# Kernel tuning notes

Hardware: AMD Instinct MI355X
Metric: run time of the kernel (lower is better)

The kernel has to match this reference:

```python
import jax, jax.numpy as jnp
import numpy as np

L0, L1, L2 = 32, 16, 8          # multiplicities of 0e, 1o, 2e irreps
NS = 128                        # numscalars
NB = 64                         # numbasis
CUTOFF = 7.0
N_NODES = 50000
N_EDGES = 400000
N_GRAPH = 32
NODE_DIM = L0 + 3 * L1 + 5 * L2  # 120


def setup_inputs() -> dict:
    key = jax.random.key(0)
    ks = jax.random.split(key, 16)
    return {
        "nodes": jax.random.normal(ks[0], (N_NODES, NODE_DIM), jnp.float32),
        "edge_index": jax.random.randint(ks[1], (2, N_EDGES), 0, N_NODES),
        "graph_batch": jnp.sort(jax.random.randint(ks[2], (N_NODES,), 0, N_GRAPH)),
        "cell": jax.random.normal(ks[3], (N_GRAPH, 3, 3), jnp.float32),
        "edge_shift": jax.random.normal(ks[4], (N_EDGES, 3), jnp.float32),
        "pos": jax.random.normal(ks[5], (N_NODES, 3), jnp.float32),
        # FullyConnectedTensorProduct weights: one uvw block per (l,l)->0e path
        "W0": jax.random.normal(ks[6], (L0, L0, NS), jnp.float32),
        "W1": jax.random.normal(ks[7], (L1, L1, NS), jnp.float32),
        "W2": jax.random.normal(ks[8], (L2, L2, NS), jnp.float32),
        "ln_g": jnp.ones((NS,), jnp.float32),
        "ln_b": jnp.zeros((NS,), jnp.float32),
        "df_w1": jax.random.normal(ks[9], (NB, 128), jnp.float32) / np.sqrt(NB).astype(np.float32),
        "df_b1": jnp.zeros((128,), jnp.float32),
        "df_w2": jax.random.normal(ks[10], (128, NS), jnp.float32) / np.sqrt(128.0).astype(np.float32),
        "df_b2": jnp.zeros((NS,), jnp.float32),
        "mlp_w1": jax.random.normal(ks[11], (NS, 512), jnp.float32) / np.sqrt(NS).astype(np.float32),
        "mlp_b1": jnp.zeros((512,), jnp.float32),
        "mlp_w2": jax.random.normal(ks[12], (512, 1), jnp.float32) / np.sqrt(512.0).astype(np.float32),
        "mlp_b2": jnp.zeros((1,), jnp.float32),
    }


def _split_irreps(x):
    # x: [E, L0 + 3*L1 + 5*L2] -> scalar / vector / rank-2 blocks
    a = x[:, :L0]                                   # [E, L0]    0e
    b = x[:, L0:L0 + 3 * L1].reshape(-1, L1, 3)     # [E, L1, 3] 1o
    c = x[:, L0 + 3 * L1:].reshape(-1, L2, 5)       # [E, L2, 5] 2e
    return a, b, c


def _tensor_product(x1, x2, W0, W1, W2):
    # e3nn FullyConnectedTensorProduct to {NS}x0e: only (l,l)->0 paths survive.
    # Real-basis wigner_3j(l,l,0) = I / sqrt(2l+1); 'element' path norm with
    # scalar output gives alpha = 1 / (L0^2 + L1^2 + L2^2) shared by all paths.
    a1, b1, c1 = _split_irreps(x1)
    a2, b2, c2 = _split_irreps(x2)
    alpha = 1.0 / np.sqrt(float(L0 * L0 + L1 * L1 + L2 * L2))
    out = (jnp.einsum('eu,ev,uvw->ew', a1, a2, W0)
           + jnp.einsum('eum,evm,uvw->ew', b1, b2, W1) * (1.0 / np.sqrt(3.0))
           + jnp.einsum('eum,evm,uvw->ew', c1, c2, W2) * (1.0 / np.sqrt(5.0)))
    return jnp.asarray(alpha, out.dtype) * out


def reference(nodes, edge_index, graph_batch, cell, edge_shift, pos,
              W0, W1, W2, ln_g, ln_b, df_w1, df_b1, df_w2, df_b2,
              mlp_w1, mlp_b1, mlp_w2, mlp_b2):
    src, dst = edge_index[0], edge_index[1]
    bcell = cell[graph_batch[src]]                            # [E,3,3]
    tvec = jnp.einsum('ei,eij->ej', edge_shift, bcell)        # [E,3]
    radvec = pos[dst] - pos[src] + tvec
    dist = jnp.linalg.norm(radvec, axis=1, keepdims=True)     # [E,1]

    mixed = _tensor_product(nodes[src], nodes[dst], W0, W1, W2)  # [E,NS]
    mu = jnp.mean(mixed, axis=-1, keepdims=True)
    var = jnp.mean((mixed - mu) ** 2, axis=-1, keepdims=True)
    mixednorm = (mixed - mu) / jnp.sqrt(var + 1e-5) * ln_g + ln_b

    # RadialEmbedding: Gaussian RBF * cosine envelope with hard cutoff
    offset = jnp.linspace(0.0, CUTOFF, NB).astype(dist.dtype)
    width = CUTOFF / (NB - 1)
    coeff = -0.5 / (width * width)
    rbf = jnp.exp(coeff * (dist - offset[None, :]) ** 2)      # [E,NB]
    env = 0.5 * (jnp.cos(dist * jnp.pi / CUTOFF) + 1.0)
    env = env * (dist < CUTOFF).astype(dist.dtype)            # [E,1]
    demb = rbf * env

    dfilter = jax.nn.silu(demb @ df_w1 + df_b1) @ df_w2 + df_b2  # [E,NS]
    regulated = mixednorm * dfilter
    out = jax.nn.silu(regulated @ mlp_w1 + mlp_b1) @ mlp_w2 + mlp_b2  # [E,1]
    return out
```

## Files before the change

kernel.cpp:

```cpp
#include <hip/hip_runtime.h>
#include <hip/hip_bf16.h>
#include <math.h>

typedef unsigned short ushort_t;
typedef short short8 __attribute__((ext_vector_type(8)));
typedef float f32x4 __attribute__((ext_vector_type(4)));

#define E_TOTAL 400000
#define ET 32
#define NTHR 512
#define NODE_D 120
#define XSTR 124

#define ALPHA 0.0272772362793f
#define S_L1  0.57735026918962f
#define S_L2  0.44721359549996f

#define WS_WF1 172032
#define WS_WF2 180224
#define WS_WM1 196608
#define WS_TOTAL 262144

__device__ __forceinline__ ushort_t f2b(float f) {
    unsigned int b = __float_as_uint(f);
    b += 0x7FFFu + ((b >> 16) & 1u);
    return (ushort_t)(b >> 16);
}
__device__ __forceinline__ unsigned int f2b2(float a, float b) {
    __hip_bfloat162 h = __float22bfloat162_rn(make_float2(a, b));
    union { __hip_bfloat162 h2; unsigned int u; } cv; cv.h2 = h;
    return cv.u;
}
__device__ __forceinline__ float silu_f(float x) { return x / (1.0f + __expf(-x)); }

__global__ __launch_bounds__(256) void prep_weights(
    const float* __restrict__ W0, const float* __restrict__ W1, const float* __restrict__ W2,
    const float* __restrict__ df_w1, const float* __restrict__ df_w2,
    const float* __restrict__ mlp_w1, ushort_t* __restrict__ ws)
{
    const int i = blockIdx.x * 256 + threadIdx.x;
    if (i >= WS_TOTAL) return;
    float v;
    if (i < WS_WF1) {
        const int r = i;
        const int kt = r >> 12, nt = (r >> 9) & 7, l = (r >> 3) & 63, jj = r & 7;
        const int k = kt * 32 + ((l >> 4) << 3) + jj;
        const int n = nt * 16 + (l & 15);
        if (k < 1024)      v = W0[k * 128 + n] * ALPHA;
        else if (k < 1280) v = W1[(k - 1024) * 128 + n] * (ALPHA * S_L1);
        else               v = W2[(k - 1280) * 128 + n] * (ALPHA * S_L2);
    } else if (i < WS_WF2) {
        const int r = i - WS_WF1;
        const int kt = r >> 12, nt = (r >> 9) & 7, l = (r >> 3) & 63, jj = r & 7;
        v = df_w1[(kt * 32 + ((l >> 4) << 3) + jj) * 128 + nt * 16 + (l & 15)];
    } else if (i < WS_WM1) {
        const int r = i - WS_WF2;
        const int kt = r >> 12, nt = (r >> 9) & 7, l = (r >> 3) & 63, jj = r & 7;
        v = df_w2[(kt * 32 + ((l >> 4) << 3) + jj) * 128 + nt * 16 + (l & 15)];
    } else {
        const int r = i - WS_WM1;
        const int kt = r >> 14, nt = (r >> 9) & 31, l = (r >> 3) & 63, jj = r & 7;
        v = mlp_w1[(kt * 32 + ((l >> 4) << 3) + jj) * 512 + nt * 16 + (l & 15)];
    }
    ws[i] = f2b(v);
}

__device__ __forceinline__ void build_l0_frag(ushort_t* __restrict__ Pf,
                                              const float* __restrict__ x1,
                                              const float* __restrict__ x2,
                                              int tid, int ubase)
{
    const int er = tid & 15, kg = (tid >> 4) & 3, w = tid >> 6;
#pragma unroll
    for (int half = 0; half < 2; ++half) {
        const int e = half * 16 + er;
        const float* x2r = x2 + e * XSTR + kg * 8;
        const float2 xv0 = *(const float2*)(x2r + 0);
        const float2 xv1 = *(const float2*)(x2r + 2);
        const float2 xv2 = *(const float2*)(x2r + 4);
        const float2 xv3 = *(const float2*)(x2r + 6);
#pragma unroll
        for (int uu = 0; uu < 2; ++uu) {
            const int ul = w + uu * 8;
            const float a1 = x1[e * XSTR + ubase + ul];
            uint4 o;
            o.x = f2b2(a1 * xv0.x, a1 * xv0.y);
            o.y = f2b2(a1 * xv1.x, a1 * xv1.y);
            o.z = f2b2(a1 * xv2.x, a1 * xv2.y);
            o.w = f2b2(a1 * xv3.x, a1 * xv3.y);
            *(uint4*)(Pf + ((ul * 2 + half) * 64 + kg * 16 + er) * 8) = o;
        }
    }
}

__global__ __launch_bounds__(NTHR, 4) void fused_edge_kernel(
    const float* __restrict__ nodes, const int* __restrict__ edge_index,
    const int* __restrict__ graph_batch, const float* __restrict__ cell,
    const float* __restrict__ edge_shift, const float* __restrict__ pos,
    const float* __restrict__ ln_g, const float* __restrict__ ln_b,
    const float* __restrict__ df_b1, const float* __restrict__ df_b2,
    const float* __restrict__ mlp_b1, const float* __restrict__ mlp_w2,
    const float* __restrict__ mlp_b2,
    const ushort_t* __restrict__ wsp, float* __restrict__ out)
{
    __shared__ __align__(16) ushort_t Pf[16 * 2 * 64 * 8];
    __shared__ __align__(16) float xbuf[2 * ET * XSTR];
    __shared__ __align__(16) ushort_t dembF[2 * 2 * 64 * 8];
    __shared__ float dist_s[ET];
    __shared__ int sidx[ET], didx[ET];
    __shared__ float mu_s[ET], rstd_s[ET];

    float* x1 = xbuf;
    float* x2 = xbuf + ET * XSTR;
    ushort_t* h1F  = (ushort_t*)xbuf;
    ushort_t* regF = (ushort_t*)xbuf + 4096;
    float* red1 = (float*)((char*)xbuf + 16384);
    float* red2 = (float*)((char*)xbuf + 18432);

    const int tid = threadIdx.x;
    const int e0g = blockIdx.x * ET;
    const int wave = tid >> 6, lane = tid & 63;
    const int lr = lane & 15, lg = lane >> 4;

    if (tid < ET) {
        const int e = e0g + tid;
        const int s = edge_index[e];
        const int d = edge_index[E_TOTAL + e];
        sidx[tid] = s; didx[tid] = d;
        const int g = graph_batch[s];
        const float* c = cell + g * 9;
        const float sx = edge_shift[e * 3], sy = edge_shift[e * 3 + 1], sz = edge_shift[e * 3 + 2];
        const float t0 = sx * c[0] + sy * c[3] + sz * c[6];
        const float t1 = sx * c[1] + sy * c[4] + sz * c[7];
        const float t2 = sx * c[2] + sy * c[5] + sz * c[8];
        const float r0 = pos[d * 3 + 0] - pos[s * 3 + 0] + t0;
        const float r1 = pos[d * 3 + 1] - pos[s * 3 + 1] + t1;
        const float r2 = pos[d * 3 + 2] - pos[s * 3 + 2] + t2;
        dist_s[tid] = sqrtf(r0 * r0 + r1 * r1 + r2 * r2);
    }
    __syncthreads();

    for (int i = tid; i < ET * 32; i += NTHR) {
        const int e = i >> 5, c = i & 31;
        if (c < 30)
            *(float4*)(x1 + e * XSTR + c * 4) = *(const float4*)(nodes + (size_t)sidx[e] * NODE_D + c * 4);
    }
    for (int i = tid; i < ET * 32; i += NTHR) {
        const int e = i >> 5, c = i & 31;
        if (c < 30)
            *(float4*)(x2 + e * XSTR + c * 4) = *(const float4*)(nodes + (size_t)didx[e] * NODE_D + c * 4);
    }
    for (int i = tid; i < ET * 64; i += NTHR) {
        const int e = i >> 6, k = i & 63;
        const float d = dist_s[e];
        const float t = d - (7.0f / 63.0f) * (float)k;
        const float rbf = __expf(-40.5f * t * t);
        const float env = (d < 7.0f) ? (0.5f * (__cosf(d * (3.14159265358979f / 7.0f)) + 1.0f)) : 0.0f;
        const int ktl = k >> 5, kg = (k >> 3) & 3, jj = k & 7, half = e >> 4, row = e & 15;
        dembF[((ktl * 2 + half) * 64 + kg * 16 + row) * 8 + jj] = f2b(rbf * env);
    }
    __syncthreads();

    const char* pA = (const char*)Pf + lane * 16;
    const short8* WT8 = (const short8*)wsp;
    const int bcol = wave * 64 + lane;

    f32x4 acc0 = {0.f, 0.f, 0.f, 0.f}, acc1 = {0.f, 0.f, 0.f, 0.f};

    build_l0_frag(Pf, x1, x2, tid, 0);
    __syncthreads();
#pragma unroll 4
    for (int kt = 0; kt < 16; ++kt) {
        const short8 a0 = *(const short8*)(pA + kt * 2048);
        const short8 a1 = *(const short8*)(pA + kt * 2048 + 1024);
        const short8 b = WT8[kt * 512 + bcol];
        acc0 = __builtin_amdgcn_mfma_f32_16x16x32_bf16(a0, b, acc0, 0, 0, 0);
        acc1 = __builtin_amdgcn_mfma_f32_16x16x32_bf16(a1, b, acc1, 0, 0, 0);
    }
    __syncthreads();

    build_l0_frag(Pf, x1, x2, tid, 16);
    __syncthreads();
#pragma unroll 4
    for (int kt = 0; kt < 16; ++kt) {
        const short8 a0 = *(const short8*)(pA + kt * 2048);
        const short8 a1 = *(const short8*)(pA + kt * 2048 + 1024);
        const short8 b = WT8[(16 + kt) * 512 + bcol];
        acc0 = __builtin_amdgcn_mfma_f32_16x16x32_bf16(a0, b, acc0, 0, 0, 0);
        acc1 = __builtin_amdgcn_mfma_f32_16x16x32_bf16(a1, b, acc1, 0, 0, 0);
    }
    __syncthreads();

    {
        const int er = tid & 15, kg = (tid >> 4) & 3, w = tid >> 6;
        const int u1 = 2 * w + (kg >> 1);
        const int vb = (kg & 1) * 8;
#pragma unroll
        for (int half = 0; half < 2; ++half) {
            const int e = half * 16 + er;
            const float* b1p = x1 + e * XSTR + 32 + 3 * u1;
            const float b1a = b1p[0], b1b = b1p[1], b1c = b1p[2];
            const float* b2b = x2 + e * XSTR + 32 + 3 * vb;
            float pr[8];
#pragma unroll
            for (int jj = 0; jj < 8; ++jj) {
                const float* b2p = b2b + 3 * jj;
                pr[jj] = b1a * b2p[0] + b1b * b2p[1] + b1c * b2p[2];
            }
            uint4 o;
            o.x = f2b2(pr[0], pr[1]); o.y = f2b2(pr[2], pr[3]);
            o.z = f2b2(pr[4], pr[5]); o.w = f2b2(pr[6], pr[7]);
            *(uint4*)(Pf + ((w * 2 + half) * 64 + lane) * 8) = o;
        }
        if (w < 4) {
            const int half = w & 1;
            const int ktl = 8 + (w >> 1);
            const int u2 = (ktl - 8) * 4 + kg;
            const int e = half * 16 + er;
            const float* c1p = x1 + e * XSTR + 80 + 5 * u2;
            const float c1a = c1p[0], c1b = c1p[1], c1c = c1p[2], c1d = c1p[3], c1e = c1p[4];
            float pr[8];
#pragma unroll
            for (int jj = 0; jj < 8; ++jj) {
                const float* c2p = x2 + e * XSTR + 80 + 5 * jj;
                pr[jj] = c1a * c2p[0] + c1b * c2p[1] + c1c * c2p[2] + c1d * c2p[3] + c1e * c2p[4];
            }
            uint4 o;
            o.x = f2b2(pr[0], pr[1]); o.y = f2b2(pr[2], pr[3]);
            o.z = f2b2(pr[4], pr[5]); o.w = f2b2(pr[6], pr[7]);
            *(uint4*)(Pf + ((ktl * 2 + half) * 64 + lane) * 8) = o;
        }
    }
    __syncthreads();

#pragma unroll 2
    for (int kt = 0; kt < 10; ++kt) {
        const short8 a0 = *(const short8*)(pA + kt * 2048);
        const short8 a1 = *(const short8*)(pA + kt * 2048 + 1024);
        const short8 b = WT8[(32 + kt) * 512 + bcol];
        acc0 = __builtin_amdgcn_mfma_f32_16x16x32_bf16(a0, b, acc0, 0, 0, 0);
        acc1 = __builtin_amdgcn_mfma_f32_16x16x32_bf16(a1, b, acc1, 0, 0, 0);
    }
    {
        f32x4 f0 = {0.f, 0.f, 0.f, 0.f}, f1 = {0.f, 0.f, 0.f, 0.f};
        const char* dA = (const char*)dembF + lane * 16;
#pragma unroll
        for (int kt = 0; kt < 2; ++kt) {
            const short8 a0 = *(const short8*)(dA + kt * 2048);
            const short8 a1 = *(const short8*)(dA + kt * 2048 + 1024);
            const short8 b = WT8[WS_WF1 / 8 + kt * 512 + bcol];
            f0 = __builtin_amdgcn_mfma_f32_16x16x32_bf16(a0, b, f0, 0, 0, 0);
            f1 = __builtin_amdgcn_mfma_f32_16x16x32_bf16(a1, b, f1, 0, 0, 0);
        }
        const int n = wave * 16 + lr;
        const float bb = df_b1[n];
        const int ktl = n >> 5, kg2 = (n >> 3) & 3, jj = n & 7;
#pragma unroll
        for (int r = 0; r < 4; ++r) {
            const int row = lg * 4 + r;
            h1F[((ktl * 2 + 0) * 64 + kg2 * 16 + row) * 8 + jj] = f2b(silu_f(f0[r] + bb));
            h1F[((ktl * 2 + 1) * 64 + kg2 * 16 + row) * 8 + jj] = f2b(silu_f(f1[r] + bb));
        }
    }
    __syncthreads();

    f32x4 d0 = {0.f, 0.f, 0.f, 0.f}, d1 = {0.f, 0.f, 0.f, 0.f};
    {
        const char* hA = (const char*)h1F + lane * 16;
#pragma unroll
        for (int kt = 0; kt < 4; ++kt) {
            const short8 a0 = *(const short8*)(hA + kt * 2048);
            const short8 a1 = *(const short8*)(hA + kt * 2048 + 1024);
            const short8 b = WT8[WS_WF2 / 8 + kt * 512 + bcol];
            d0 = __builtin_amdgcn_mfma_f32_16x16x32_bf16(a0, b, d0, 0, 0, 0);
            d1 = __builtin_amdgcn_mfma_f32_16x16x32_bf16(a1, b, d1, 0, 0, 0);
        }
        const int n = wave * 16 + lr;
        const float b2v = df_b2[n];
#pragma unroll
        for (int r = 0; r < 4; ++r) { d0[r] += b2v; d1[r] += b2v; }
    }
#pragma unroll
    for (int mt = 0; mt < 2; ++mt) {
#pragma unroll
        for (int r = 0; r < 4; ++r) {
            const float v = mt ? acc1[r] : acc0[r];
            float s1 = v, s2 = v * v;
            s1 += __shfl_xor(s1, 1);  s2 += __shfl_xor(s2, 1);
            s1 += __shfl_xor(s1, 2);  s2 += __shfl_xor(s2, 2);
            s1 += __shfl_xor(s1, 4);  s2 += __shfl_xor(s2, 4);
            s1 += __shfl_xor(s1, 8);  s2 += __shfl_xor(s2, 8);
            if (lr == 0) {
                const int idx = ((wave * 2 + mt) * 4 + lg) * 4 + r;
                red1[idx] = s1;
                red1[256 + idx] = s2;
            }
        }
    }
    __syncthreads();
    if (tid < ET) {
        const int mt = tid >> 4, g = (tid >> 2) & 3, r = tid & 3;
        float s1 = 0.f, s2 = 0.f;
#pragma unroll
        for (int w = 0; w < 8; ++w) {
            const int idx = ((w * 2 + mt) * 4 + g) * 4 + r;
            s1 += red1[idx];
            s2 += red1[256 + idx];
        }
        const float mu = s1 * (1.0f / 128.0f);
        const float var = s2 * (1.0f / 128.0f) - mu * mu;
        mu_s[tid] = mu;
        rstd_s[tid] = rsqrtf(var + 1e-5f);
    }
    __syncthreads();

    {
        const int n = wave * 16 + lr;
        const float gv = ln_g[n], bv = ln_b[n];
        const int ktl = n >> 5, kg2 = (n >> 3) & 3, jj = n & 7;
#pragma unroll
        for (int mt = 0; mt < 2; ++mt) {
#pragma unroll
            for (int r = 0; r < 4; ++r) {
                const int row = lg * 4 + r;
                const float v = mt ? acc1[r] : acc0[r];
                const float ln = (v - mu_s[mt * 16 + row]) * rstd_s[mt * 16 + row] * gv + bv;
                const float df = mt ? d1[r] : d0[r];
                regF[((ktl * 2 + mt) * 64 + kg2 * 16 + row) * 8 + jj] = f2b(ln * df);
            }
        }
    }
    __syncthreads();

    {
        f32x4 m00 = {0.f,0.f,0.f,0.f}, m01 = {0.f,0.f,0.f,0.f};
        f32x4 m10 = {0.f,0.f,0.f,0.f}, m11 = {0.f,0.f,0.f,0.f};
        f32x4 m20 = {0.f,0.f,0.f,0.f}, m21 = {0.f,0.f,0.f,0.f};
        f32x4 m30 = {0.f,0.f,0.f,0.f}, m31 = {0.f,0.f,0.f,0.f};
        const char* rA = (const char*)regF + lane * 16;
#pragma unroll
        for (int kt = 0; kt < 4; ++kt) {
            const short8 a0 = *(const short8*)(rA + kt * 2048);
            const short8 a1 = *(const short8*)(rA + kt * 2048 + 1024);
            const int base = WS_WM1 / 8 + kt * 2048 + wave * 256 + lane;
            const short8 b0 = WT8[base];
            const short8 b1 = WT8[base + 64];
            const short8 b2 = WT8[base + 128];
            const short8 b3 = WT8[base + 192];
            m00 = __builtin_amdgcn_mfma_f32_16x16x32_bf16(a0, b0, m00, 0, 0, 0);
            m01 = __builtin_amdgcn_mfma_f32_16x16x32_bf16(a1, b0, m01, 0, 0, 0);
            m10 = __builtin_amdgcn_mfma_f32_16x16x32_bf16(a0, b1, m10, 0, 0, 0);
            m11 = __builtin_amdgcn_mfma_f32_16x16x32_bf16(a1, b1, m11, 0, 0, 0);
            m20 = __builtin_amdgcn_mfma_f32_16x16x32_bf16(a0, b2, m20, 0, 0, 0);
            m21 = __builtin_amdgcn_mfma_f32_16x16x32_bf16(a1, b2, m21, 0, 0, 0);
            m30 = __builtin_amdgcn_mfma_f32_16x16x32_bf16(a0, b3, m30, 0, 0, 0);
            m31 = __builtin_amdgcn_mfma_f32_16x16x32_bf16(a1, b3, m31, 0, 0, 0);
        }
        float po0[4] = {0.f,0.f,0.f,0.f}, po1[4] = {0.f,0.f,0.f,0.f};
#pragma unroll
        for (int q = 0; q < 4; ++q) {
            const int n = (wave * 4 + q) * 16 + lr;
            const float b1v = mlp_b1[n];
            const float w2v = mlp_w2[n];
            const f32x4 h0 = (q == 0) ? m00 : (q == 1) ? m10 : (q == 2) ? m20 : m30;
            const f32x4 h1v = (q == 0) ? m01 : (q == 1) ? m11 : (q == 2) ? m21 : m31;
#pragma unroll
            for (int r = 0; r < 4; ++r) {
                po0[r] += silu_f(h0[r] + b1v) * w2v;
                po1[r] += silu_f(h1v[r] + b1v) * w2v;
            }
        }
#pragma unroll
        for (int r = 0; r < 4; ++r) {
            float a = po0[r], b = po1[r];
            a += __shfl_xor(a, 1); b += __shfl_xor(b, 1);
            a += __shfl_xor(a, 2); b += __shfl_xor(b, 2);
            a += __shfl_xor(a, 4); b += __shfl_xor(b, 4);
            a += __shfl_xor(a, 8); b += __shfl_xor(b, 8);
            if (lr == 0) {
                red2[((wave * 2 + 0) * 4 + lg) * 4 + r] = a;
                red2[((wave * 2 + 1) * 4 + lg) * 4 + r] = b;
            }
        }
    }
    __syncthreads();
    if (tid < ET) {
        const int mt = tid >> 4, g = (tid >> 2) & 3, r = tid & 3;
        float s = 0.f;
#pragma unroll
        for (int w = 0; w < 8; ++w)
            s += red2[((w * 2 + mt) * 4 + g) * 4 + r];
        out[e0g + tid] = s + mlp_b2[0];
    }
}

extern "C" void kernel_launch(void* const* d_in, const int* in_sizes, int n_in,
                              void* d_out, int out_size, void* d_ws, size_t ws_size,
                              hipStream_t stream) {
    const float* nodes      = (const float*)d_in[0];
    const int*   edge_index = (const int*)  d_in[1];
    const int*   graph_b    = (const int*)  d_in[2];
    const float* cell       = (const float*)d_in[3];
    const float* edge_shift = (const float*)d_in[4];
    const float* pos        = (const float*)d_in[5];
    const float* W0         = (const float*)d_in[6];
    const float* W1         = (const float*)d_in[7];
    const float* W2         = (const float*)d_in[8];
    const float* ln_g       = (const float*)d_in[9];
    const float* ln_b       = (const float*)d_in[10];
    const float* df_w1      = (const float*)d_in[11];
    const float* df_b1      = (const float*)d_in[12];
    const float* df_w2      = (const float*)d_in[13];
    const float* df_b2      = (const float*)d_in[14];
    const float* mlp_w1     = (const float*)d_in[15];
    const float* mlp_b1     = (const float*)d_in[16];
    const float* mlp_w2     = (const float*)d_in[17];
    const float* mlp_b2     = (const float*)d_in[18];
    float* out = (float*)d_out;
    ushort_t* ws = (ushort_t*)d_ws;

    hipLaunchKernelGGL(prep_weights, dim3((WS_TOTAL + 255) / 256), dim3(256), 0, stream,
                       W0, W1, W2, df_w1, df_w2, mlp_w1, ws);

    const int E = in_sizes[1] / 2;
    const int grid = E / ET;
    hipLaunchKernelGGL(fused_edge_kernel, dim3(grid), dim3(NTHR), 0, stream,
                       nodes, edge_index, graph_b, cell, edge_shift, pos,
                       ln_g, ln_b, df_b1, df_b2, mlp_b1, mlp_w2, mlp_b2,
                       ws, out);
}
```

Measured before the change: 509.4 us.

## Process 64 edges per block and stage irrep gathers to reuse weight fragments

Doubles the edges per workgroup from 32 to 64, so each B-fragment loaded from the weight workspace feeds four MFMA row tiles instead of two. The l=0 tensor-product chunks are rebuilt in four passes, with the destination scalars kept in registers across passes. The 1o/2e node slices are gathered late, during the last l=0 pass, so shared memory stays small. This halves the global weight traffic per edge. In exchange it raises register pressure (16 MLP accumulators per thread, cached float2s) and shared-memory use, which may lower occupancy. Launch grid code presumably also changes to E/64 blocks.

Result: faster. 458.2 us (-10.1%).

```diff
diff --git a/kernel.cpp b/kernel.cpp
--- a/kernel.cpp
+++ b/kernel.cpp
@@ -7,10 +7,11 @@
 typedef float f32x4 __attribute__((ext_vector_type(4)));
 
 #define E_TOTAL 400000
-#define ET 32
+#define ET 64
 #define NTHR 512
 #define NODE_D 120
-#define XSTR 124
+#define ASTR 36
+#define BCSTR 92
 
 #define ALPHA 0.0272772362793f
 #define S_L1  0.57735026918962f
@@ -65,34 +66,6 @@
     ws[i] = f2b(v);
 }
 
-__device__ __forceinline__ void build_l0_frag(ushort_t* __restrict__ Pf,
-                                              const float* __restrict__ x1,
-                                              const float* __restrict__ x2,
-                                              int tid, int ubase)
-{
-    const int er = tid & 15, kg = (tid >> 4) & 3, w = tid >> 6;
-#pragma unroll
-    for (int half = 0; half < 2; ++half) {
-        const int e = half * 16 + er;
-        const float* x2r = x2 + e * XSTR + kg * 8;
-        const float2 xv0 = *(const float2*)(x2r + 0);
-        const float2 xv1 = *(const float2*)(x2r + 2);
-        const float2 xv2 = *(const float2*)(x2r + 4);
-        const float2 xv3 = *(const float2*)(x2r + 6);
-#pragma unroll
-        for (int uu = 0; uu < 2; ++uu) {
-            const int ul = w + uu * 8;
-            const float a1 = x1[e * XSTR + ubase + ul];
-            uint4 o;
-            o.x = f2b2(a1 * xv0.x, a1 * xv0.y);
-            o.y = f2b2(a1 * xv1.x, a1 * xv1.y);
-            o.z = f2b2(a1 * xv2.x, a1 * xv2.y);
-            o.w = f2b2(a1 * xv3.x, a1 * xv3.y);
-            *(uint4*)(Pf + ((ul * 2 + half) * 64 + kg * 16 + er) * 8) = o;
-        }
-    }
-}
-
 __global__ __launch_bounds__(NTHR, 4) void fused_edge_kernel(
     const float* __restrict__ nodes, const int* __restrict__ edge_index,
     const int* __restrict__ graph_batch, const float* __restrict__ cell,
@@ -103,24 +76,27 @@
     const float* __restrict__ mlp_b2,
     const ushort_t* __restrict__ wsp, float* __restrict__ out)
 {
-    __shared__ __align__(16) ushort_t Pf[16 * 2 * 64 * 8];
-    __shared__ __align__(16) float xbuf[2 * ET * XSTR];
-    __shared__ __align__(16) ushort_t dembF[2 * 2 * 64 * 8];
+    __shared__ __align__(16) ushort_t Pf[8 * 4 * 64 * 8];
+    __shared__ __align__(16) char Xb[47104];
     __shared__ float dist_s[ET];
     __shared__ int sidx[ET], didx[ET];
     __shared__ float mu_s[ET], rstd_s[ET];
 
-    float* x1 = xbuf;
-    float* x2 = xbuf + ET * XSTR;
-    ushort_t* h1F  = (ushort_t*)xbuf;
-    ushort_t* regF = (ushort_t*)xbuf + 4096;
-    float* red1 = (float*)((char*)xbuf + 16384);
-    float* red2 = (float*)((char*)xbuf + 18432);
+    float* xa1 = (float*)Xb;
+    float* xa2 = xa1 + ET * ASTR;
+    float* bc1 = (float*)Xb;
+    float* bc2 = bc1 + ET * BCSTR;
+    ushort_t* h1F  = (ushort_t*)Xb;
+    ushort_t* regF = h1F + 8192;
+    float* red1 = (float*)(Xb + 32768);
+    float* red2 = (float*)(Xb + 36864);
+    ushort_t* dembF = Pf + 4096;
 
     const int tid = threadIdx.x;
     const int e0g = blockIdx.x * ET;
     const int wave = tid >> 6, lane = tid & 63;
     const int lr = lane & 15, lg = lane >> 4;
+    const int er = tid & 15, kg = (tid >> 4) & 3, w = tid >> 6;
 
     if (tid < ET) {
         const int e = e0g + tid;
@@ -140,15 +116,122 @@
     }
     __syncthreads();
 
-    for (int i = tid; i < ET * 32; i += NTHR) {
-        const int e = i >> 5, c = i & 31;
-        if (c < 30)
-            *(float4*)(x1 + e * XSTR + c * 4) = *(const float4*)(nodes + (size_t)sidx[e] * NODE_D + c * 4);
-    }
-    for (int i = tid; i < ET * 32; i += NTHR) {
-        const int e = i >> 5, c = i & 31;
-        if (c < 30)
-            *(float4*)(x2 + e * XSTR + c * 4) = *(const float4*)(nodes + (size_t)didx[e] * NODE_D + c * 4);
+    {
+        const int e = tid >> 3, c = tid & 7;
+        *(float4*)(xa1 + e * ASTR + c * 4) = *(const float4*)(nodes + (size_t)sidx[e] * NODE_D + c * 4);
+        *(float4*)(xa2 + e * ASTR + c * 4) = *(const float4*)(nodes + (size_t)didx[e] * NODE_D + c * 4);
+    }
+    __syncthreads();
+
+    const char* pA = (const char*)Pf + lane * 16;
+    const short8* WT8 = (const short8*)wsp;
+    const int bcol = tid;
+
+    f32x4 acc[4] = {{0.f,0.f,0.f,0.f},{0.f,0.f,0.f,0.f},{0.f,0.f,0.f,0.f},{0.f,0.f,0.f,0.f}};
+
+    float2 a2v[4][4];
+#pragma unroll
+    for (int h = 0; h < 4; ++h)
+#pragma unroll
+        for (int q = 0; q < 4; ++q)
+            a2v[h][q] = *(const float2*)(xa2 + (h * 16 + er) * ASTR + kg * 8 + q * 2);
+
+#pragma unroll 1
+    for (int c4 = 0; c4 < 4; ++c4) {
+#pragma unroll
+        for (int h = 0; h < 4; ++h) {
+            const float a1 = xa1[(h * 16 + er) * ASTR + c4 * 8 + w];
+            uint4 o;
+            o.x = f2b2(a1 * a2v[h][0].x, a1 * a2v[h][0].y);
+            o.y = f2b2(a1 * a2v[h][1].x, a1 * a2v[h][1].y);
+            o.z = f2b2(a1 * a2v[h][2].x, a1 * a2v[h][2].y);
+            o.w = f2b2(a1 * a2v[h][3].x, a1 * a2v[h][3].y);
+            *(uint4*)(Pf + ((w * 4 + h) * 64 + kg * 16 + er) * 8) = o;
+        }
+        __syncthreads();
+#pragma unroll 2
+        for (int kt = 0; kt < 8; ++kt) {
+            const short8 b = WT8[(c4 * 8 + kt) * 512 + bcol];
+#pragma unroll
+            for (int h = 0; h < 4; ++h) {
+                const short8 a = *(const short8*)(pA + (kt * 4 + h) * 1024);
+                acc[h] = __builtin_amdgcn_mfma_f32_16x16x32_bf16(a, b, acc[h], 0, 0, 0);
+            }
+        }
+        if (c4 == 3) {
+            for (int i = tid; i < ET * 22; i += NTHR) {
+                const int e = i / 22, c = i % 22;
+                *(float4*)(bc1 + e * BCSTR + c * 4) =
+                    *(const float4*)(nodes + (size_t)sidx[e] * NODE_D + 32 + c * 4);
+            }
+            for (int i = tid; i < ET * 22; i += NTHR) {
+                const int e = i / 22, c = i % 22;
+                *(float4*)(bc2 + e * BCSTR + c * 4) =
+                    *(const float4*)(nodes + (size_t)didx[e] * NODE_D + 32 + c * 4);
+            }
+        }
+        __syncthreads();
+    }
+
+    {
+        const int u1 = 2 * w + (kg >> 1);
+        const int vb = (kg & 1) * 8;
+#pragma unroll
+        for (int h = 0; h < 4; ++h) {
+            const int e = h * 16 + er;
+            const float* b1p = bc1 + e * BCSTR + 3 * u1;
+            const float b1a = b1p[0], b1b = b1p[1], b1c = b1p[2];
+            const float* b2b = bc2 + e * BCSTR + 3 * vb;
+            float pr[8];
+#pragma unroll
+            for (int jj = 0; jj < 8; ++jj) {
+                const float* b2p = b2b + 3 * jj;
+                pr[jj] = b1a * b2p[0] + b1b * b2p[1] + b1c * b2p[2];
+            }
+            uint4 o;
+            o.x = f2b2(pr[0], pr[1]); o.y = f2b2(pr[2], pr[3]);
+            o.z = f2b2(pr[4], pr[5]); o.w = f2b2(pr[6], pr[7]);
+            *(uint4*)(Pf + ((w * 4 + h) * 64 + kg * 16 + er) * 8) = o;
+        }
+    }
+    __syncthreads();
+#pragma unroll 2
+    for (int kt = 0; kt < 8; ++kt) {
+        const short8 b = WT8[(32 + kt) * 512 + bcol];
+#pragma unroll
+        for (int h = 0; h < 4; ++h) {
+            const short8 a = *(const short8*)(pA + (kt * 4 + h) * 1024);
+            acc[h] = __builtin_amdgcn_mfma_f32_16x16x32_bf16(a, b, acc[h], 0, 0, 0);
+        }
+    }
+    __syncthreads();
+
+    {
+        const int ktl = w >> 2, h2 = w & 3;
+        const int u2 = ktl * 4 + kg;
+        const int e = h2 * 16 + er;
+        const float* c1p = bc1 + e * BCSTR + 48 + 5 * u2;
+        const float c1a = c1p[0], c1b = c1p[1], c1c = c1p[2], c1d = c1p[3], c1e = c1p[4];
+        float pr[8];
+#pragma unroll
+        for (int jj = 0; jj < 8; ++jj) {
+            const float* c2p = bc2 + e * BCSTR + 48 + 5 * jj;
+            pr[jj] = c1a * c2p[0] + c1b * c2p[1] + c1c * c2p[2] + c1d * c2p[3] + c1e * c2p[4];
+        }
+        uint4 o;
+        o.x = f2b2(pr[0], pr[1]); o.y = f2b2(pr[2], pr[3]);
+        o.z = f2b2(pr[4], pr[5]); o.w = f2b2(pr[6], pr[7]);
+        *(uint4*)(Pf + ((ktl * 4 + h2) * 64 + kg * 16 + er) * 8) = o;
+    }
+    __syncthreads();
+#pragma unroll
+    for (int kt = 0; kt < 2; ++kt) {
+        const short8 b = WT8[(40 + kt) * 512 + bcol];
+#pragma unroll
+        for (int h = 0; h < 4; ++h) {
+            const short8 a = *(const short8*)(pA + (kt * 4 + h) * 1024);
+            acc[h] = __builtin_amdgcn_mfma_f32_16x16x32_bf16(a, b, acc[h], 0, 0, 0);
+        }
     }
     for (int i = tid; i < ET * 64; i += NTHR) {
         const int e = i >> 6, k = i & 63;
@@ -156,156 +239,79 @@
         const float t = d - (7.0f / 63.0f) * (float)k;
         const float rbf = __expf(-40.5f * t * t);
         const float env = (d < 7.0f) ? (0.5f * (__cosf(d * (3.14159265358979f / 7.0f)) + 1.0f)) : 0.0f;
-        const int ktl = k >> 5, kg = (k >> 3) & 3, jj = k & 7, half = e >> 4, row = e & 15;
-        dembF[((ktl * 2 + half) * 64 + kg * 16 + row) * 8 + jj] = f2b(rbf * env);
-    }
-    __syncthreads();
-
-    const char* pA = (const char*)Pf + lane * 16;
-    const short8* WT8 = (const short8*)wsp;
-    const int bcol = wave * 64 + lane;
-
-    f32x4 acc0 = {0.f, 0.f, 0.f, 0.f}, acc1 = {0.f, 0.f, 0.f, 0.f};
-
-    build_l0_frag(Pf, x1, x2, tid, 0);
-    __syncthreads();
-#pragma unroll 4
-    for (int kt = 0; kt < 16; ++kt) {
-        const short8 a0 = *(const short8*)(pA + kt * 2048);
-        const short8 a1 = *(const short8*)(pA + kt * 2048 + 1024);
-        const short8 b = WT8[kt * 512 + bcol];
-        acc0 = __builtin_amdgcn_mfma_f32_16x16x32_bf16(a0, b, acc0, 0, 0, 0);
-        acc1 = __builtin_amdgcn_mfma_f32_16x16x32_bf16(a1, b, acc1, 0, 0, 0);
-    }
-    __syncthreads();
-
-    build_l0_frag(Pf, x1, x2, tid, 16);
-    __syncthreads();
-#pragma unroll 4
-    for (int kt = 0; kt < 16; ++kt) {
-        const short8 a0 = *(const short8*)(pA + kt * 2048);
-        const short8 a1 = *(const short8*)(pA + kt * 2048 + 1024);
-        const short8 b = WT8[(16 + kt) * 512 + bcol];
-        acc0 = __builtin_amdgcn_mfma_f32_16x16x32_bf16(a0, b, acc0, 0, 0, 0);
-        acc1 = __builtin_amdgcn_mfma_f32_16x16x32_bf16(a1, b, acc1, 0, 0, 0);
-    }
-    __syncthreads();
-
-    {
-        const int er = tid & 15, kg = (tid >> 4) & 3, w = tid >> 6;
-        const int u1 = 2 * w + (kg >> 1);
-        const int vb = (kg & 1) * 8;
-#pragma unroll
-        for (int half = 0; half < 2; ++half) {
-            const int e = half * 16 + er;
-            const float* b1p = x1 + e * XSTR + 32 + 3 * u1;
-            const float b1a = b1p[0], b1b = b1p[1], b1c = b1p[2];
-            const float* b2b = x2 + e * XSTR + 32 + 3 * vb;
-            float pr[8];
-#pragma unroll
-            for (int jj = 0; jj < 8; ++jj) {
-                const float* b2p = b2b + 3 * jj;
-                pr[jj] = b1a * b2p[0] + b1b * b2p[1] + b1c * b2p[2];
-            }
-            uint4 o;
-            o.x = f2b2(pr[0], pr[1]); o.y = f2b2(pr[2], pr[3]);
-            o.z = f2b2(pr[4], pr[5]); o.w = f2b2(pr[6], pr[7]);
-            *(uint4*)(Pf + ((w * 2 + half) * 64 + lane) * 8) = o;
-        }
-        if (w < 4) {
-            const int half = w & 1;
-            const int ktl = 8 + (w >> 1);
-            const int u2 = (ktl - 8) * 4 + kg;
-            const int e = half * 16 + er;
-            const float* c1p = x1 + e * XSTR + 80 + 5 * u2;
-            const float c1a = c1p[0], c1b = c1p[1], c1c = c1p[2], c1d = c1p[3], c1e = c1p[4];
-            float pr[8];
-#pragma unroll
-            for (int jj = 0; jj < 8; ++jj) {
-                const float* c2p = x2 + e * XSTR + 80 + 5 * jj;
-                pr[jj] = c1a * c2p[0] + c1b * c2p[1] + c1c * c2p[2] + c1d * c2p[3] + c1e * c2p[4];
-            }
-            uint4 o;
-            o.x = f2b2(pr[0], pr[1]); o.y = f2b2(pr[2], pr[3]);
-            o.z = f2b2(pr[4], pr[5]); o.w = f2b2(pr[6], pr[7]);
-            *(uint4*)(Pf + ((ktl * 2 + half) * 64 + lane) * 8) = o;
-        }
-    }
-    __syncthreads();
-
-#pragma unroll 2
-    for (int kt = 0; kt < 10; ++kt) {
-        const short8 a0 = *(const short8*)(pA + kt * 2048);
-        const short8 a1 = *(const short8*)(pA + kt * 2048 + 1024);
-        const short8 b = WT8[(32 + kt) * 512 + bcol];
-        acc0 = __builtin_amdgcn_mfma_f32_16x16x32_bf16(a0, b, acc0, 0, 0, 0);
-        acc1 = __builtin_amdgcn_mfma_f32_16x16x32_bf16(a1, b, acc1, 0, 0, 0);
-    }
-    {
-        f32x4 f0 = {0.f, 0.f, 0.f, 0.f}, f1 = {0.f, 0.f, 0.f, 0.f};
+        const int ktl = k >> 5, kgd = (k >> 3) & 3, jj = k & 7, half = e >> 4, row = e & 15;
+        dembF[((ktl * 4 + half) * 64 + kgd * 16 + row) * 8 + jj] = f2b(rbf * env);
+    }
+    __syncthreads();
+
+    {
+        f32x4 f[4] = {{0.f,0.f,0.f,0.f},{0.f,0.f,0.f,0.f},{0.f,0.f,0.f,0.f},{0.f,0.f,0.f,0.f}};
         const char* dA = (const char*)dembF + lane * 16;
 #pragma unroll
         for (int kt = 0; kt < 2; ++kt) {
-            const short8 a0 = *(const short8*)(dA + kt * 2048);
-            const short8 a1 = *(const short8*)(dA + kt * 2048 + 1024);
             const short8 b = WT8[WS_WF1 / 8 + kt * 512 + bcol];
-            f0 = __builtin_amdgcn_mfma_f32_16x16x32_bf16(a0, b, f0, 0, 0, 0);
-            f1 = __builtin_amdgcn_mfma_f32_16x16x32_bf16(a1, b, f1, 0, 0, 0);
+#pragma unroll
+            for (int h = 0; h < 4; ++h) {
+                const short8 a = *(const short8*)(dA + (kt * 4 + h) * 1024);
+                f[h] = __builtin_amdgcn_mfma_f32_16x16x32_bf16(a, b, f[h], 0, 0, 0);
+            }
         }
         const int n = wave * 16 + lr;
         const float bb = df_b1[n];
-        const int ktl = n >> 5, kg2 = (n >> 3) & 3, jj = n & 7;
-#pragma unroll
-        for (int r = 0; r < 4; ++r) {
-            const int row = lg * 4 + r;
-            h1F[((ktl * 2 + 0) * 64 + kg2 * 16 + row) * 8 + jj] = f2b(silu_f(f0[r] + bb));
-            h1F[((ktl * 2 + 1) * 64 + kg2 * 16 + row) * 8 + jj] = f2b(silu_f(f1[r] + bb));
-        }
-    }
-    __syncthreads();
-
-    f32x4 d0 = {0.f, 0.f, 0.f, 0.f}, d1 = {0.f, 0.f, 0.f, 0.f};
+        const int ktl = n >> 5, kg2 = (n >> 3) & 3, jjn = n & 7;
+#pragma unroll
+        for (int h = 0; h < 4; ++h)
+#pragma unroll
+            for (int r = 0; r < 4; ++r)
+                h1F[((ktl * 4 + h) * 64 + kg2 * 16 + lg * 4 + r) * 8 + jjn] = f2b(silu_f(f[h][r] + bb));
+    }
+    __syncthreads();
+
+    f32x4 d[4] = {{0.f,0.f,0.f,0.f},{0.f,0.f,0.f,0.f},{0.f,0.f,0.f,0.f},{0.f,0.f,0.f,0.f}};
     {
         const char* hA = (const char*)h1F + lane * 16;
 #pragma unroll
         for (int kt = 0; kt < 4; ++kt) {
-            const short8 a0 = *(const short8*)(hA + kt * 2048);
-            const short8 a1 = *(const short8*)(hA + kt * 2048 + 1024);
             const short8 b = WT8[WS_WF2 / 8 + kt * 512 + bcol];
-            d0 = __builtin_amdgcn_mfma_f32_16x16x32_bf16(a0, b, d0, 0, 0, 0);
-            d1 = __builtin_amdgcn_mfma_f32_16x16x32_bf16(a1, b, d1, 0, 0, 0);
+#pragma unroll
+            for (int h = 0; h < 4; ++h) {
+                const short8 a = *(const short8*)(hA + (kt * 4 + h) * 1024);
+                d[h] = __builtin_amdgcn_mfma_f32_16x16x32_bf16(a, b, d[h], 0, 0, 0);
+            }
         }
         const int n = wave * 16 + lr;
         const float b2v = df_b2[n];
 #pragma unroll
-        for (int r = 0; r < 4; ++r) { d0[r] += b2v; d1[r] += b2v; }
-    }
-#pragma unroll
-    for (int mt = 0; mt < 2; ++mt) {
+        for (int h = 0; h < 4; ++h)
+#pragma unroll
+            for (int r = 0; r < 4; ++r) d[h][r] += b2v;
+    }
+#pragma unroll
+    for (int h = 0; h < 4; ++h) {
 #pragma unroll
         for (int r = 0; r < 4; ++r) {
-            const float v = mt ? acc1[r] : acc0[r];
+            const float v = acc[h][r];
             float s1 = v, s2 = v * v;
             s1 += __shfl_xor(s1, 1);  s2 += __shfl_xor(s2, 1);
             s1 += __shfl_xor(s1, 2);  s2 += __shfl_xor(s2, 2);
             s1 += __shfl_xor(s1, 4);  s2 += __shfl_xor(s2, 4);
             s1 += __shfl_xor(s1, 8);  s2 += __shfl_xor(s2, 8);
             if (lr == 0) {
-                const int idx = ((wave * 2 + mt) * 4 + lg) * 4 + r;
+                const int idx = ((wave * 4 + h) * 4 + lg) * 4 + r;
                 red1[idx] = s1;
-                red1[256 + idx] = s2;
+                red1[512 + idx] = s2;
             }
         }
     }
     __syncthreads();
     if (tid < ET) {
-        const int mt = tid >> 4, g = (tid >> 2) & 3, r = tid & 3;
+        const int h = tid >> 4, g = (tid >> 2) & 3, r = tid & 3;
         float s1 = 0.f, s2 = 0.f;
 #pragma unroll
-        for (int w = 0; w < 8; ++w) {
-            const int idx = ((w * 2 + mt) * 4 + g) * 4 + r;
+        for (int ww = 0; ww < 8; ++ww) {
+            const int idx = ((ww * 4 + h) * 4 + g) * 4 + r;
             s1 += red1[idx];
-            s2 += red1[256 + idx];
+            s2 += red1[512 + idx];
         }
         const float mu = s1 * (1.0f / 128.0f);
         const float var = s2 * (1.0f / 128.0f) - mu * mu;
@@ -317,79 +323,77 @@
     {
         const int n = wave * 16 + lr;
         const float gv = ln_g[n], bv = ln_b[n];
-        const int ktl = n >> 5, kg2 = (n >> 3) & 3, jj = n & 7;
-#pragma unroll
-        for (int mt = 0; mt < 2; ++mt) {
+        const int ktl = n >> 5, kg2 = (n >> 3) & 3, jjn = n & 7;
+#pragma unroll
+        for (int h = 0; h < 4; ++h) {
 #pragma unroll
             for (int r = 0; r < 4; ++r) {
-                const int row = lg * 4 + r;
-                const float v = mt ? acc1[r] : acc0[r];
-                const float ln = (v - mu_s[mt * 16 + row]) * rstd_s[mt * 16 + row] * gv + bv;
-                const float df = mt ? d1[r] : d0[r];
-                regF[((ktl * 2 + mt) * 64 + kg2 * 16 + row) * 8 + jj] = f2b(ln * df);
-            }
-        }
-    }
-    __syncthreads();
-
-    {
-        f32x4 m00 = {0.f,0.f,0.f,0.f}, m01 = {0.f,0.f,0.f,0.f};
-        f32x4 m10 = {0.f,0.f,0.f,0.f}, m11 = {0.f,0.f,0.f,0.f};
-        f32x4 m20 = {0.f,0.f,0.f,0.f}, m21 = {0.f,0.f,0.f,0.f};
-        f32x4 m30 = {0.f,0.f,0.f,0.f}, m31 = {0.f,0.f,0.f,0.f};
+                const int row = lg * 4 + r, e = h * 16 + row;
+                const float ln = (acc[h][r] - mu_s[e]) * rstd_s[e] * gv + bv;
+                regF[((ktl * 4 + h) * 64 + kg2 * 16 + row) * 8 + jjn] = f2b(ln * d[h][r]);
+            }
+        }
+    }
+    __syncthreads();
+
+    {
+        f32x4 m[4][4];
+#pragma unroll
+        for (int q = 0; q < 4; ++q)
+#pragma unroll
+            for (int h = 0; h < 4; ++h) m[q][h] = (f32x4){0.f,0.f,0.f,0.f};
         const char* rA = (const char*)regF + lane * 16;
 #pragma unroll
         for (int kt = 0; kt < 4; ++kt) {
-            const short8 a0 = *(const short8*)(rA + kt * 2048);
-            const short8 a1 = *(const short8*)(rA + kt * 2048 + 1024);
+            short8 a[4];
+#pragma unroll
+            for (int h = 0; h < 4; ++h)
+                a[h] = *(const short8*)(rA + (kt * 4 + h) * 1024);
             const int base = WS_WM1 / 8 + kt * 2048 + wave * 256 + lane;
-            const short8 b0 = WT8[base];
-            const short8 b1 = WT8[base + 64];
-            const short8 b2 = WT8[base + 128];
-            const short8 b3 = WT8[base + 192];
-            m00 = __builtin_amdgcn_mfma_f32_16x16x32_bf16(a0, b0, m00, 0, 0, 0);
-            m01 = __builtin_amdgcn_mfma_f32_16x16x32_bf16(a1, b0, m01, 0, 0, 0);
-            m10 = __builtin_amdgcn_mfma_f32_16x16x32_bf16(a0, b1, m10, 0, 0, 0);
-            m11 = __builtin_amdgcn_mfma_f32_16x16x32_bf16(a1, b1, m11, 0, 0, 0);
-            m20 = __builtin_amdgcn_mfma_f32_16x16x32_bf16(a0, b2, m20, 0, 0, 0);
-            m21 = __builtin_amdgcn_mfma_f32_16x16x32_bf16(a1, b2, m21, 0, 0, 0);
-            m30 = __builtin_amdgcn_mfma_f32_16x16x32_bf16(a0, b3, m30, 0, 0, 0);
-            m31 = __builtin_amdgcn_mfma_f32_16x16x32_bf16(a1, b3, m31, 0, 0, 0);
-        }
-        float po0[4] = {0.f,0.f,0.f,0.f}, po1[4] = {0.f,0.f,0.f,0.f};
+#pragma unroll
+            for (int q = 0; q < 4; ++q) {
+                const short8 b = WT8[base + q * 64];
+#pragma unroll
+                for (int h = 0; h < 4; ++h)
+                    m[q][h] = __builtin_amdgcn_mfma_f32_16x16x32_bf16(a[h], b, m[q][h], 0, 0, 0);
+            }
+        }
+        float po[4][4];
+#pragma unroll
+        for (int h = 0; h < 4; ++h)
+#pragma unroll
+            for (int r = 0; r < 4; ++r) po[h][r] = 0.f;
 #pragma unroll
         for (int q = 0; q < 4; ++q) {
             const int n = (wave * 4 + q) * 16 + lr;
             const float b1v = mlp_b1[n];
             const float w2v = mlp_w2[n];
-            const f32x4 h0 = (q == 0) ? m00 : (q == 1) ? m10 : (q == 2) ? m20 : m30;
-            const f32x4 h1v = (q == 0) ? m01 : (q == 1) ? m11 : (q == 2) ? m21 : m31;
+#pragma unroll
+            for (int h = 0; h < 4; ++h)
+#pragma unroll
+                for (int r = 0; r < 4; ++r)
+                    po[h][r] += silu_f(m[q][h][r] + b1v) * w2v;
+        }
+#pragma unroll
+        for (int h = 0; h < 4; ++h) {
 #pragma unroll
             for (int r = 0; r < 4; ++r) {
-                po0[r] += silu_f(h0[r] + b1v) * w2v;
-                po1[r] += silu_f(h1v[r] + b1v) * w2v;
-            }
-        }
-#pragma unroll
-        for (int r = 0; r < 4; ++r) {
-            float a = po0[r], b = po1[r];
-            a += __shfl_xor(a, 1); b += __shfl_xor(b, 1);
-            a += __shfl_xor(a, 2); b += __shfl_xor(b, 2);
-            a += __shfl_xor(a, 4); b += __shfl_xor(b, 4);
-            a += __shfl_xor(a, 8); b += __shfl_xor(b, 8);
-            if (lr == 0) {
-                red2[((wave * 2 + 0) * 4 + lg) * 4 + r] = a;
-                red2[((wave * 2 + 1) * 4 + lg) * 4 + r] = b;
+                float a = po[h][r];
+                a += __shfl_xor(a, 1);
+                a += __shfl_xor(a, 2);
+                a += __shfl_xor(a, 4);
+                a += __shfl_xor(a, 8);
+                if (lr == 0) red2[((wave * 4 + h) * 4 + lg) * 4 + r] = a;
             }
         }
     }
     __syncthreads();
     if (tid < ET) {
-        const int mt = tid >> 4, g = (tid >> 2) & 3, r = tid & 3;
+        const int h = tid >> 4, g = (tid >> 2) & 3, r = tid & 3;
         float s = 0.f;
 #pragma unroll
-        for (int w = 0; w < 8; ++w)
-            s += red2[((w * 2 + mt) * 4 + g) * 4 + r];
+        for (int ww = 0; ww < 8; ++ww)
+            s += red2[((ww * 4 + h) * 4 + g) * 4 + r];
         out[e0g + tid] = s + mlp_b2[0];
     }
 }
```
